# Kernel tuning notes

Hardware: AMD Instinct MI355X
Metric: run time of the kernel (lower is better)

## Reference

```python
import jax, jax.numpy as jnp
import numpy as np

B, C, N, K = 8, 192, 3136, 9
OUT_CH = 192
BN_EPS = 1e-5


def setup_inputs() -> dict:
    key = jax.random.key(0)
    k1, k2, k3, k4 = jax.random.split(key, 4)
    x = jax.random.normal(k1, (B, C, N, 1), dtype=jnp.float32)
    y = jax.random.normal(k2, (B, C, N, 1), dtype=jnp.float32)
    edge_index = jax.random.randint(k3, (2, B, N, K), 0, N, dtype=jnp.int64)
    # 1x1 conv weight (out_ch, in_ch*2), no bias (BatchNorm follows)
    W = jax.random.normal(k4, (OUT_CH, 2 * C), dtype=jnp.float32) / np.sqrt(2 * C)
    gamma = jnp.ones((OUT_CH,), dtype=jnp.float32)
    beta = jnp.zeros((OUT_CH,), dtype=jnp.float32)
    return {"x": x, "y": y, "edge_index": edge_index, "W": W, "gamma": gamma, "beta": beta}


def _gather(feat, idx):
    # feat: (B, C, N); idx: (B, M, K) -> (B, C, M, K)
    return jax.vmap(lambda f, i: f[:, i])(feat, idx)


def reference(x, y, edge_index, W, gamma, beta):
    xt = x[..., 0]  # (B, C, N)
    yt = y[..., 0]
    x_i = _gather(xt, edge_index[1])          # (B, C, N, K)
    x_j = _gather(yt, edge_index[0])          # (B, C, N, K)
    rel = jnp.max(x_j - x_i, axis=-1, keepdims=True)  # (B, C, N, 1)
    h = jnp.concatenate([x, rel], axis=1)     # (B, 2C, N, 1)
    # 1x1 conv
    out = jnp.einsum('oc,bcnk->bonk', W, h)   # (B, out_ch, N, 1)
    # BatchNorm2d (training-mode batch statistics)
    mean = out.mean(axis=(0, 2, 3), keepdims=True)
    var = out.var(axis=(0, 2, 3), keepdims=True)
    out = (out - mean) * jax.lax.rsqrt(var + BN_EPS)
    out = out * gamma[None, :, None, None] + beta[None, :, None, None]
    return jax.nn.gelu(out, approximate=False)
```

## Files before the change

### kernel.cpp

```cpp
#include <hip/hip_runtime.h>
#include <hip/hip_bf16.h>

#define B_    8
#define C_    192
#define N_    3136
#define K_    9
#define OC    192
#define KDIM  384
#define ROWS  (B_ * N_)
#define BNK   (B_ * N_ * K_)

typedef __hip_bfloat16 bf16;
using short8 = __attribute__((ext_vector_type(8))) short;
using f32x4  = __attribute__((ext_vector_type(4))) float;

__device__ inline float bf2f(bf16 v) { return __bfloat162float(v); }
__device__ inline bf16  f2bf(float v) { return __float2bfloat16(v); }

__global__ void k_transpose(const float* __restrict__ x, const float* __restrict__ y,
                            bf16* __restrict__ h, bf16* __restrict__ yT) {
    __shared__ float tile[32][33];
    int tx = threadIdx.x, ty = threadIdx.y;
    int n0 = blockIdx.x * 32, c0 = blockIdx.y * 32;
    int bz = blockIdx.z;
    int b = bz >> 1, which = bz & 1;
    const float* src = which ? y : x;
#pragma unroll
    for (int i = 0; i < 4; i++) {
        int c = c0 + ty + i * 8;
        tile[ty + i * 8][tx] = src[((size_t)b * C_ + c) * N_ + n0 + tx];
    }
    __syncthreads();
    if (which == 0) {
#pragma unroll
        for (int i = 0; i < 4; i++) {
            int n = n0 + ty + i * 8;
            h[((size_t)b * N_ + n) * KDIM + c0 + tx] = f2bf(tile[tx][ty + i * 8]);
        }
    } else {
#pragma unroll
        for (int i = 0; i < 4; i++) {
            int n = n0 + ty + i * 8;
            yT[((size_t)b * N_ + n) * C_ + c0 + tx] = f2bf(tile[tx][ty + i * 8]);
        }
    }
}

__global__ void k_wprep(const float* __restrict__ W, bf16* __restrict__ Wb) {
    int i = blockIdx.x * 256 + threadIdx.x;
    if (i < OC * KDIM) Wb[i] = f2bf(W[i]);
}

__global__ void k_gather_rel(const int* __restrict__ ei, bf16* __restrict__ h,
                             const bf16* __restrict__ yT) {
    int wave = threadIdx.x >> 6;
    int lane = threadIdx.x & 63;
    int r = blockIdx.x * 4 + wave;
    int b = r / N_;

    const int* e0 = ei + (size_t)r * K_;
    const int* e1 = ei + (size_t)BNK + (size_t)r * K_;
    int ej[K_], eii[K_];
#pragma unroll
    for (int k = 0; k < K_; k++) { ej[k] = e0[k]; eii[k] = e1[k]; }

    const bf16* ybase = yT + (size_t)b * N_ * C_;
    const bf16* xbase = h + (size_t)b * N_ * KDIM;

#pragma unroll
    for (int ch = 0; ch < 3; ch++) {
        int c = ch * 64 + lane;
        float m = -3.4e38f;
#pragma unroll
        for (int k = 0; k < K_; k++) {
            float vy = bf2f(ybase[(size_t)ej[k] * C_ + c]);
            float vx = bf2f(xbase[(size_t)eii[k] * KDIM + c]);
            m = fmaxf(m, vy - vx);
        }
        h[(size_t)r * KDIM + C_ + c] = f2bf(m);
    }
}

__launch_bounds__(192)
__global__ void k_gemm(const bf16* __restrict__ h, const bf16* __restrict__ Wb,
                       float* __restrict__ outp, float* __restrict__ stats) {
    int tid = threadIdx.x;
    int wave = tid >> 6, lane = tid & 63;
    int fcol = lane & 15, fgrp = lane >> 4;
    int r0 = blockIdx.x * 64;
    int colbase = wave * 64;

    f32x4 acc[4][4] = {};

    for (int kk = 0; kk < 12; kk++) {
        short8 a[4], bb[4];
#pragma unroll
        for (int i = 0; i < 4; i++)
            a[i] = *reinterpret_cast<const short8*>(
                h + (size_t)(r0 + i * 16 + fcol) * KDIM + kk * 32 + fgrp * 8);
#pragma unroll
        for (int j = 0; j < 4; j++)
            bb[j] = *reinterpret_cast<const short8*>(
                Wb + (size_t)(colbase + j * 16 + fcol) * KDIM + kk * 32 + fgrp * 8);
#pragma unroll
        for (int i = 0; i < 4; i++)
#pragma unroll
            for (int j = 0; j < 4; j++)
                acc[i][j] = __builtin_amdgcn_mfma_f32_16x16x32_bf16(a[i], bb[j], acc[i][j], 0, 0, 0);
    }

#pragma unroll
    for (int j = 0; j < 4; j++) {
        int o = colbase + j * 16 + fcol;
        float s1 = 0.f, s2 = 0.f;
#pragma unroll
        for (int i = 0; i < 4; i++) {
            int rbase = r0 + i * 16 + fgrp * 4;
#pragma unroll
            for (int e = 0; e < 4; e++) {
                float v = acc[i][j][e];
                outp[(size_t)(rbase + e) * OC + o] = v;
                s1 += v;
                s2 += v * v;
            }
        }
        s1 += __shfl_xor(s1, 16); s1 += __shfl_xor(s1, 32);
        s2 += __shfl_xor(s2, 16); s2 += __shfl_xor(s2, 32);
        if (fgrp == 0) {
            atomicAdd(&stats[o], s1);
            atomicAdd(&stats[OC + o], s2);
        }
    }
}

__global__ void k_bn_gelu(const float* __restrict__ outp, const float* __restrict__ stats,
                          const float* __restrict__ gamma, const float* __restrict__ beta,
                          float* __restrict__ out) {
    __shared__ float tile[32][33];
    int tx = threadIdx.x, ty = threadIdx.y;
    int n0 = blockIdx.x * 32, o0 = blockIdx.y * 32, b = blockIdx.z;
#pragma unroll
    for (int i = 0; i < 4; i++) {
        int n = n0 + ty + i * 8;
        tile[ty + i * 8][tx] = outp[(size_t)(b * N_ + n) * OC + o0 + tx];
    }
    __syncthreads();
    const float invc = 1.0f / (float)ROWS;
#pragma unroll
    for (int i = 0; i < 4; i++) {
        int o = o0 + ty + i * 8;
        float mean = stats[o] * invc;
        float var  = stats[OC + o] * invc - mean * mean;
        float is   = rsqrtf(var + 1e-5f);
        float g = gamma[o], bt = beta[o];
        float v = tile[tx][ty + i * 8];
        float z = (v - mean) * is * g + bt;
        float gl = 0.5f * z * (1.0f + erff(z * 0.70710678118654752f));
        out[((size_t)b * OC + o) * N_ + n0 + tx] = gl;
    }
}

extern "C" void kernel_launch(void* const* d_in, const int* in_sizes, int n_in,
                              void* d_out, int out_size, void* d_ws, size_t ws_size,
                              hipStream_t stream) {
    const float* x     = (const float*)d_in[0];
    const float* y     = (const float*)d_in[1];
    const int*   ei    = (const int*)d_in[2];
    const float* W     = (const float*)d_in[3];
    const float* gamma = (const float*)d_in[4];
    const float* beta  = (const float*)d_in[5];
    float* out = (float*)d_out;

    char* ws = (char*)d_ws;
    bf16*  h     = (bf16*)(ws);
    bf16*  yT    = (bf16*)(ws + 19267584);
    bf16*  Wb    = (bf16*)(ws + 19267584 + 9633792);
    float* outp  = (float*)(ws + 29048832);
    float* stats = (float*)(ws + 48316416);

    hipMemsetAsync(stats, 0, 2 * OC * sizeof(float), stream);

    dim3 bt(32, 8);
    k_transpose<<<dim3(N_ / 32, C_ / 32, 2 * B_), bt, 0, stream>>>(x, y, h, yT);
    k_wprep<<<(OC * KDIM + 255) / 256, 256, 0, stream>>>(W, Wb);
    k_gather_rel<<<ROWS / 4, 256, 0, stream>>>(ei, h, yT);
    k_gemm<<<ROWS / 64, 192, 0, stream>>>(h, Wb, outp, stats);
    k_bn_gelu<<<dim3(N_ / 32, OC / 32, B_), bt, 0, stream>>>(outp, stats, gamma, beta, out);
}
```

Baseline: 153.9 us.

## Recompute GEMM for BN+GELU epilogue, drop intermediate buffer, fuse prep kernels

```diff
diff --git a/kernel.cpp b/kernel.cpp
--- a/kernel.cpp
+++ b/kernel.cpp
@@ -12,17 +12,38 @@
 
 typedef __hip_bfloat16 bf16;
 using short8 = __attribute__((ext_vector_type(8))) short;
+using us4    = __attribute__((ext_vector_type(4))) unsigned short;
 using f32x4  = __attribute__((ext_vector_type(4))) float;
 
-__device__ inline float bf2f(bf16 v) { return __bfloat162float(v); }
-__device__ inline bf16  f2bf(float v) { return __float2bfloat16(v); }
-
-__global__ void k_transpose(const float* __restrict__ x, const float* __restrict__ y,
-                            bf16* __restrict__ h, bf16* __restrict__ yT) {
+__device__ inline float bfbits2f(unsigned short u) {
+    unsigned int x = ((unsigned int)u) << 16;
+    return __builtin_bit_cast(float, x);
+}
+__device__ inline bf16 f2bf(float v) { return __float2bfloat16(v); }
+__device__ inline unsigned short f2bfbits(float v) {
+    bf16 t = __float2bfloat16(v);
+    return *reinterpret_cast<unsigned short*>(&t);
+}
+
+__global__ void k_prep(const float* __restrict__ x, const float* __restrict__ y,
+                       const float* __restrict__ W,
+                       bf16* __restrict__ h, bf16* __restrict__ yT,
+                       bf16* __restrict__ Wb, float* __restrict__ stats) {
+    int tx = threadIdx.x, ty = threadIdx.y;
+    int bz = blockIdx.z;
+    if (bz == 16) {
+        int flat = blockIdx.y * 98 + blockIdx.x;
+        int t = ty * 32 + tx;
+        if (flat < 288) {
+            int i = flat * 256 + t;
+            Wb[i] = f2bf(W[i]);
+        }
+        if (flat == 0) stats[t] = 0.f;
+        if (flat == 1 && t < 128) stats[256 + t] = 0.f;
+        return;
+    }
     __shared__ float tile[32][33];
-    int tx = threadIdx.x, ty = threadIdx.y;
     int n0 = blockIdx.x * 32, c0 = blockIdx.y * 32;
-    int bz = blockIdx.z;
     int b = bz >> 1, which = bz & 1;
     const float* src = which ? y : x;
 #pragma unroll
@@ -44,11 +65,6 @@
             yT[((size_t)b * N_ + n) * C_ + c0 + tx] = f2bf(tile[tx][ty + i * 8]);
         }
     }
-}
-
-__global__ void k_wprep(const float* __restrict__ W, bf16* __restrict__ Wb) {
-    int i = blockIdx.x * 256 + threadIdx.x;
-    if (i < OC * KDIM) Wb[i] = f2bf(W[i]);
 }
 
 __global__ void k_gather_rel(const int* __restrict__ ei, bf16* __restrict__ h,
@@ -64,26 +80,30 @@
 #pragma unroll
     for (int k = 0; k < K_; k++) { ej[k] = e0[k]; eii[k] = e1[k]; }
 
-    const bf16* ybase = yT + (size_t)b * N_ * C_;
-    const bf16* xbase = h + (size_t)b * N_ * KDIM;
-
-#pragma unroll
-    for (int ch = 0; ch < 3; ch++) {
-        int c = ch * 64 + lane;
-        float m = -3.4e38f;
+    const us4* y4 = (const us4*)(yT + (size_t)b * N_ * C_);
+    const us4* x4 = (const us4*)(h + (size_t)b * N_ * KDIM);
+
+    if (lane < 48) {
+        float m0 = -3.4e38f, m1 = -3.4e38f, m2 = -3.4e38f, m3 = -3.4e38f;
 #pragma unroll
         for (int k = 0; k < K_; k++) {
-            float vy = bf2f(ybase[(size_t)ej[k] * C_ + c]);
-            float vx = bf2f(xbase[(size_t)eii[k] * KDIM + c]);
-            m = fmaxf(m, vy - vx);
-        }
-        h[(size_t)r * KDIM + C_ + c] = f2bf(m);
+            us4 vy = y4[(size_t)ej[k] * 48 + lane];
+            us4 vx = x4[(size_t)eii[k] * 96 + lane];
+            m0 = fmaxf(m0, bfbits2f(vy.x) - bfbits2f(vx.x));
+            m1 = fmaxf(m1, bfbits2f(vy.y) - bfbits2f(vx.y));
+            m2 = fmaxf(m2, bfbits2f(vy.z) - bfbits2f(vx.z));
+            m3 = fmaxf(m3, bfbits2f(vy.w) - bfbits2f(vx.w));
+        }
+        us4 o;
+        o.x = f2bfbits(m0); o.y = f2bfbits(m1);
+        o.z = f2bfbits(m2); o.w = f2bfbits(m3);
+        *((us4*)(h + (size_t)r * KDIM + C_) + lane) = o;
     }
 }
 
 __launch_bounds__(192)
-__global__ void k_gemm(const bf16* __restrict__ h, const bf16* __restrict__ Wb,
-                       float* __restrict__ outp, float* __restrict__ stats) {
+__global__ void k_gemm_stats(const bf16* __restrict__ h, const bf16* __restrict__ Wb,
+                             float* __restrict__ stats) {
     int tid = threadIdx.x;
     int wave = tid >> 6, lane = tid & 63;
     int fcol = lane & 15, fgrp = lane >> 4;
@@ -114,16 +134,13 @@
         int o = colbase + j * 16 + fcol;
         float s1 = 0.f, s2 = 0.f;
 #pragma unroll
-        for (int i = 0; i < 4; i++) {
-            int rbase = r0 + i * 16 + fgrp * 4;
+        for (int i = 0; i < 4; i++)
 #pragma unroll
             for (int e = 0; e < 4; e++) {
                 float v = acc[i][j][e];
-                outp[(size_t)(rbase + e) * OC + o] = v;
                 s1 += v;
                 s2 += v * v;
             }
-        }
         s1 += __shfl_xor(s1, 16); s1 += __shfl_xor(s1, 32);
         s2 += __shfl_xor(s2, 16); s2 += __shfl_xor(s2, 32);
         if (fgrp == 0) {
@@ -133,30 +150,56 @@
     }
 }
 
-__global__ void k_bn_gelu(const float* __restrict__ outp, const float* __restrict__ stats,
+__launch_bounds__(192)
+__global__ void k_gemm_bn(const bf16* __restrict__ h, const bf16* __restrict__ Wb,
+                          const float* __restrict__ stats,
                           const float* __restrict__ gamma, const float* __restrict__ beta,
                           float* __restrict__ out) {
-    __shared__ float tile[32][33];
-    int tx = threadIdx.x, ty = threadIdx.y;
-    int n0 = blockIdx.x * 32, o0 = blockIdx.y * 32, b = blockIdx.z;
+    int tid = threadIdx.x;
+    int wave = tid >> 6, lane = tid & 63;
+    int fcol = lane & 15, fgrp = lane >> 4;
+    int r0 = blockIdx.x * 64;
+    int b = r0 / N_;
+    int n0 = r0 % N_;
+    int colbase = wave * 64;
+
+    f32x4 acc[4][4] = {};
+
+    for (int kk = 0; kk < 12; kk++) {
+        short8 wfr[4], hfr[4];
+#pragma unroll
+        for (int i = 0; i < 4; i++)
+            wfr[i] = *reinterpret_cast<const short8*>(
+                Wb + (size_t)(colbase + i * 16 + fcol) * KDIM + kk * 32 + fgrp * 8);
+#pragma unroll
+        for (int j = 0; j < 4; j++)
+            hfr[j] = *reinterpret_cast<const short8*>(
+                h + (size_t)(r0 + j * 16 + fcol) * KDIM + kk * 32 + fgrp * 8);
+#pragma unroll
+        for (int i = 0; i < 4; i++)
+#pragma unroll
+            for (int j = 0; j < 4; j++)
+                acc[i][j] = __builtin_amdgcn_mfma_f32_16x16x32_bf16(wfr[i], hfr[j], acc[i][j], 0, 0, 0);
+    }
+
+    const float invc = 1.0f / (float)ROWS;
 #pragma unroll
     for (int i = 0; i < 4; i++) {
-        int n = n0 + ty + i * 8;
-        tile[ty + i * 8][tx] = outp[(size_t)(b * N_ + n) * OC + o0 + tx];
-    }
-    __syncthreads();
-    const float invc = 1.0f / (float)ROWS;
-#pragma unroll
-    for (int i = 0; i < 4; i++) {
-        int o = o0 + ty + i * 8;
-        float mean = stats[o] * invc;
-        float var  = stats[OC + o] * invc - mean * mean;
-        float is   = rsqrtf(var + 1e-5f);
-        float g = gamma[o], bt = beta[o];
-        float v = tile[tx][ty + i * 8];
-        float z = (v - mean) * is * g + bt;
-        float gl = 0.5f * z * (1.0f + erff(z * 0.70710678118654752f));
-        out[((size_t)b * OC + o) * N_ + n0 + tx] = gl;
+#pragma unroll
+        for (int e = 0; e < 4; e++) {
+            int o = colbase + i * 16 + fgrp * 4 + e;
+            float mean = stats[o] * invc;
+            float var  = stats[OC + o] * invc - mean * mean;
+            float is   = rsqrtf(var + 1e-5f);
+            float sc = gamma[o] * is;
+            float sh = beta[o] - mean * sc;
+#pragma unroll
+            for (int j = 0; j < 4; j++) {
+                float z = acc[i][j][e] * sc + sh;
+                float gl = 0.5f * z * (1.0f + erff(z * 0.70710678118654752f));
+                out[((size_t)b * OC + o) * N_ + n0 + j * 16 + fcol] = gl;
+            }
+        }
     }
 }
 
@@ -175,15 +218,11 @@
     bf16*  h     = (bf16*)(ws);
     bf16*  yT    = (bf16*)(ws + 19267584);
     bf16*  Wb    = (bf16*)(ws + 19267584 + 9633792);
-    float* outp  = (float*)(ws + 29048832);
-    float* stats = (float*)(ws + 48316416);
-
-    hipMemsetAsync(stats, 0, 2 * OC * sizeof(float), stream);
+    float* stats = (float*)(ws + 19267584 + 9633792 + 147456);
 
     dim3 bt(32, 8);
-    k_transpose<<<dim3(N_ / 32, C_ / 32, 2 * B_), bt, 0, stream>>>(x, y, h, yT);
-    k_wprep<<<(OC * KDIM + 255) / 256, 256, 0, stream>>>(W, Wb);
+    k_prep<<<dim3(N_ / 32, C_ / 32, 2 * B_ + 1), bt, 0, stream>>>(x, y, W, h, yT, Wb, stats);
     k_gather_rel<<<ROWS / 4, 256, 0, stream>>>(ei, h, yT);
-    k_gemm<<<ROWS / 64, 192, 0, stream>>>(h, Wb, outp, stats);
-    k_bn_gelu<<<dim3(N_ / 32, OC / 32, B_), bt, 0, stream>>>(outp, stats, gamma, beta, out);
-}
+    k_gemm_stats<<<ROWS / 64, 192, 0, stream>>>(h, Wb, stats);
+    k_gemm_bn<<<ROWS / 64, 192, 0, stream>>>(h, Wb, stats, gamma, beta, out);
+}
```

After: 166.4 us. +8.1%, slower.
